# Optimization experiments

Measured on AMD Instinct MI355X. Metric: run time of the kernel, lower is better.

Reference implementation:

```python
import jax, jax.numpy as jnp
import numpy as np

B, N, DIM = 1, 2048, 2048
H, KVH = 32, 4                 # query heads, kv heads
D = DIM // H                   # head_dim = 64
REP = H // KVH                 # queries per kv = 8
KV_DIM = D * KVH               # 256


def _rope_tables(n, d, base=10000.0):
    inv = 1.0 / (base ** (np.arange(0, d, 2, dtype=np.float32) / d))
    t = np.arange(n, dtype=np.float32)
    freqs = np.outer(t, inv)                      # [n, d/2]
    emb = np.concatenate([freqs, freqs], axis=-1)  # [n, d]
    return jnp.asarray(np.cos(emb)), jnp.asarray(np.sin(emb))


def setup_inputs() -> dict:
    key = jax.random.key(0)
    ks = jax.random.split(key, 5)
    s = 0.02
    cos, sin = _rope_tables(N, D)
    return {
        "x": jax.random.normal(ks[0], (B, N, DIM), jnp.float32),
        "Wq": jax.random.normal(ks[1], (DIM, DIM), jnp.float32) * s,
        "Wk": jax.random.normal(ks[2], (KV_DIM, DIM), jnp.float32) * s,
        "Wv": jax.random.normal(ks[3], (KV_DIM, DIM), jnp.float32) * s,
        "Wo": jax.random.normal(ks[4], (DIM, DIM), jnp.float32) * s,
        "cos": cos,
        "sin": sin,
    }


def _rotate_half(t):
    d2 = t.shape[-1] // 2
    return jnp.concatenate([-t[..., d2:], t[..., :d2]], axis=-1)


def reference(x, Wq, Wk, Wv, Wo, cos, sin):
    b, n, _ = x.shape
    # projections (nn.Linear: x @ W.T)
    q = (x @ Wq.T).reshape(b, n, H, D).transpose(0, 2, 1, 3)     # b h n d
    k = (x @ Wk.T).reshape(b, n, KVH, D).transpose(0, 2, 1, 3)   # b g n d
    v = (x @ Wv.T).reshape(b, n, KVH, D).transpose(0, 2, 1, 3)
    # RoPE
    c = cos[None, None, :, :]
    s = sin[None, None, :, :]
    q = q * c + _rotate_half(q) * s
    k = k * c + _rotate_half(k) * s
    # expand KV heads (repeat_interleave over head dim)
    k = jnp.repeat(k, REP, axis=1)   # b h n d
    v = jnp.repeat(v, REP, axis=1)
    # causal attention with materialized scores (faithful to source)
    scale = 1.0 / jnp.sqrt(jnp.asarray(D, x.dtype))
    scores = jnp.einsum('bhld,bhsd->bhls', q, k) * scale
    causal = jnp.tril(jnp.ones((n, n), bool))
    scores = jnp.where(causal[None, None], scores, jnp.asarray(-jnp.inf, x.dtype))
    attn = jax.nn.softmax(scores, axis=-1)
    y = jnp.einsum('bhls,bhsd->bhld', attn, v)       # b h n d
    y = y.transpose(0, 2, 1, 3).reshape(b, n, DIM)   # b n (h d)
    return y @ Wo.T
```

## Files before the change

kernel.cpp:

```cpp
#include <hip/hip_runtime.h>

typedef unsigned short u16;
typedef __attribute__((ext_vector_type(8))) short short8;
typedef __attribute__((ext_vector_type(4))) float floatx4;

#define N_TOK 2048
#define DIM   2048
#define NH    32
#define NKVH  4
#define HD    64
#define KVD   256

#define OFF_X   0
#define OFF_WQ  4194304
#define OFF_WK  8388608
#define OFF_WV  8912896
#define OFF_WO  9437184
#define OFF_QP  13631488
#define OFF_KP  17825792
#define OFF_VP  18350080
#define OFF_YB  18874368

__device__ __forceinline__ float bf2f(u16 u) {
  union { unsigned i; float f; } c; c.i = ((unsigned)u) << 16; return c.f;
}
__device__ __forceinline__ u16 f2bf(float f) {
  union { float f; unsigned i; } c; c.f = f;
  unsigned x = c.i;
  return (u16)((x + 0x7fffu + ((x >> 16) & 1u)) >> 16);
}

__device__ __forceinline__ void gload16(const u16* g, u16* l) {
#if defined(__has_builtin) && __has_builtin(__builtin_amdgcn_global_load_lds)
  __builtin_amdgcn_global_load_lds(
      (const __attribute__((address_space(1))) void*)g,
      (__attribute__((address_space(3))) void*)l, 16, 0, 0);
#else
  *(short8*)l = *(const short8*)g;
#endif
}


__global__ __launch_bounds__(256) void cvt_pack(const float* __restrict__ x,
                                                const float* __restrict__ wq,
                                                const float* __restrict__ wk,
                                                const float* __restrict__ wv,
                                                const float* __restrict__ wo,
                                                u16* __restrict__ ws) {
  __shared__ __align__(16) u16 Ls[2048];
  const int tid = threadIdx.x;
  const int rfg = blockIdx.x >> 4;
  const int kcg = blockIdx.x & 15;
  const float* src; u16* dst; int lrf;
  if      (rfg < 128) { src = x;  dst = ws + OFF_X;  lrf = rfg; }
  else if (rfg < 256) { src = wq; dst = ws + OFF_WQ; lrf = rfg - 128; }
  else if (rfg < 272) { src = wk; dst = ws + OFF_WK; lrf = rfg - 256; }
  else if (rfg < 288) { src = wv; dst = ws + OFF_WV; lrf = rfg - 272; }
  else                { src = wo; dst = ws + OFF_WO; lrf = rfg - 288; }

  const int rr = tid >> 4, cb = tid & 15;
  const float* s = src + (size_t)(lrf * 16 + rr) * DIM + kcg * 128 + cb * 8;
  float4 v0 = ((const float4*)s)[0];
  float4 v1 = ((const float4*)s)[1];
  ushort4 o0, o1;
  o0.x = f2bf(v0.x); o0.y = f2bf(v0.y); o0.z = f2bf(v0.z); o0.w = f2bf(v0.w);
  o1.x = f2bf(v1.x); o1.y = f2bf(v1.y); o1.z = f2bf(v1.z); o1.w = f2bf(v1.w);
  const int ch = cb >> 2, qq = cb & 3;
  u16* lp = &Ls[ch * 512 + (qq * 16 + rr) * 8];
  ((ushort4*)lp)[0] = o0;
  ((ushort4*)lp)[1] = o1;
  __syncthreads();
  const int och = tid >> 6, lane = tid & 63;
  *(short8*)(dst + ((size_t)(lrf * 64 + kcg * 4 + och)) * 512 + lane * 8) =
      *(const short8*)&Ls[och * 512 + lane * 8];
}


__global__ __launch_bounds__(256) void gemm_qkv(const u16* __restrict__ xp,
                                                const u16* __restrict__ Wqp,
                                                const u16* __restrict__ Wkp,
                                                const u16* __restrict__ Wvp,
                                                const float* __restrict__ cs,
                                                const float* __restrict__ sn,
                                                u16* __restrict__ Qp,
                                                u16* __restrict__ Kp,
                                                u16* __restrict__ Vp) {
  __shared__ __align__(16) u16 As[8 * 512];
  __shared__ __align__(16) u16 Bs[16 * 512];
  const int tid  = threadIdx.x;
  const int lane = tid & 63;
  const int w    = tid >> 6;
  const int r    = lane & 15, q = lane >> 4;
  const int tm = blockIdx.x & 31;
  const int tn = blockIdx.x >> 5;
  const int wm = w & 1, wn = w >> 1;

  const u16* Wp; int rfB0;
  if (tn < 16)      { Wp = Wqp; rfB0 = tn * 8; }
  else if (tn < 18) { Wp = Wkp; rfB0 = (tn - 16) * 8; }
  else              { Wp = Wvp; rfB0 = (tn - 18) * 8; }
  const int rfA0 = tm * 4;

  const int cA0 = w, cA1 = w + 4;
  const u16* aS0 = xp + ((size_t)(rfA0 + (cA0 >> 1)) * 64 + (cA0 & 1)) * 512 + lane * 8;
  const u16* aS1 = xp + ((size_t)(rfA0 + (cA1 >> 1)) * 64 + (cA1 & 1)) * 512 + lane * 8;
  const u16* bS[4];
#pragma unroll
  for (int j = 0; j < 4; ++j) {
    int ch = w + 4 * j;
    bS[j] = Wp + ((size_t)(rfB0 + (ch >> 1)) * 64 + (ch & 1)) * 512 + lane * 8;
  }

  floatx4 acc[2][4];
#pragma unroll
  for (int a = 0; a < 2; ++a)
#pragma unroll
    for (int b = 0; b < 4; ++b) acc[a][b] = (floatx4){0.f, 0.f, 0.f, 0.f};

  for (int kc0 = 0; kc0 < 64; kc0 += 2) {
    const size_t ko = (size_t)kc0 * 512;
    __syncthreads();
    gload16(aS0 + ko, &As[cA0 * 512 + lane * 8]);
    gload16(aS1 + ko, &As[cA1 * 512 + lane * 8]);
#pragma unroll
    for (int j = 0; j < 4; ++j)
      gload16(bS[j] + ko, &Bs[(w + 4 * j) * 512 + lane * 8]);
    __syncthreads();

    short8 af[2][2], bf[4][2];
#pragma unroll
    for (int mi = 0; mi < 2; ++mi)
#pragma unroll
      for (int c = 0; c < 2; ++c)
        af[mi][c] = *(const short8*)&As[((wm * 2 + mi) * 2 + c) * 512 + lane * 8];
#pragma unroll
    for (int nj = 0; nj < 4; ++nj)
#pragma unroll
      for (int c = 0; c < 2; ++c)
        bf[nj][c] = *(const short8*)&Bs[((wn * 4 + nj) * 2 + c) * 512 + lane * 8];
#pragma unroll
    for (int c = 0; c < 2; ++c)
#pragma unroll
      for (int mi = 0; mi < 2; ++mi)
#pragma unroll
        for (int nj = 0; nj < 4; ++nj)
          acc[mi][nj] = __builtin_amdgcn_mfma_f32_16x16x32_bf16(af[mi][c], bf[nj][c], acc[mi][nj], 0, 0, 0);
  }

  if (tn < 18) {
    const int head = (tn < 16) ? (tn * 2 + wn) : ((tn - 16) * 2 + wn);
#pragma unroll
    for (int mi = 0; mi < 2; ++mi)
#pragma unroll
      for (int g = 0; g < 4; ++g) {
        int row = tm * 64 + wm * 32 + mi * 16 + 4 * q + g;
        const float* crow  = cs + (size_t)row * 64;
        const float* srow2 = sn + (size_t)row * 64;
#pragma unroll
        for (int nj = 0; nj < 2; ++nj) {
          int d = nj * 16 + r;
          float x0 = acc[mi][nj][g];
          float x1 = acc[mi][nj + 2][g];
          float o0 = x0 * crow[d]      - x1 * srow2[d];
          float o1 = x1 * crow[d + 32] + x0 * srow2[d + 32];
          int qq = d >> 3, j = d & 7;
          int lslot = (qq * 16 + (row & 15)) * 8 + j;
          if (tn < 16) {
            int sq = row >> 5, ii = (row >> 4) & 1;
            size_t base = ((size_t)(head * 64 + sq) * 4 + ii * 2) * 512 + lslot;
            Qp[base]       = f2bf(o0);
            Qp[base + 512] = f2bf(o1);
          } else {
            int kt2 = row >> 6, t = (row >> 4) & 3;
            size_t base = ((size_t)(head * 32 + kt2) * 8 + t * 2) * 512 + lslot;
            Kp[base]       = f2bf(o0);
            Kp[base + 512] = f2bf(o1);
          }
        }
      }
  } else {
#pragma unroll
    for (int mi = 0; mi < 2; ++mi)
#pragma unroll
      for (int nj = 0; nj < 4; ++nj) {
        int col  = (tn - 18) * 128 + wn * 64 + nj * 16 + r;
        int kvh  = col >> 6;
        int t    = (col & 63) >> 4;
        int rr   = col & 15;
        int row0 = tm * 64 + wm * 32 + mi * 16 + 4 * q;
        int kt2  = row0 >> 6;
        int wk   = row0 & 63;
        int s    = wk >> 5;
        int qq   = (wk & 31) >> 3;
        int j0   = wk & 7;
        uint2 pk;
        pk.x = (unsigned)f2bf(acc[mi][nj][0]) | ((unsigned)f2bf(acc[mi][nj][1]) << 16);
        pk.y = (unsigned)f2bf(acc[mi][nj][2]) | ((unsigned)f2bf(acc[mi][nj][3]) << 16);
        size_t idx = ((size_t)(kvh * 32 + kt2) * 8 + s * 4 + t) * 512 + (qq * 16 + rr) * 8 + j0;
        *(uint2*)(Vp + idx) = pk;
      }
  }
}

__global__ __launch_bounds__(256) void gemm_out(const u16* __restrict__ Ap,
                                                const u16* __restrict__ Wp,
                                                float* __restrict__ C) {
  __shared__ __align__(16) u16 As[8 * 512];
  __shared__ __align__(16) u16 Bs[16 * 512];
  const int tid  = threadIdx.x;
  const int lane = tid & 63;
  const int w    = tid >> 6;
  const int r    = lane & 15, q = lane >> 4;
  const int tn = blockIdx.x & 15;
  const int tm = blockIdx.x >> 4;
  const int wm = w & 1, wn = w >> 1;

  const int rfA0 = tm * 4, rfB0 = tn * 8;
  const int cA0 = w, cA1 = w + 4;
  const u16* aS0 = Ap + ((size_t)(rfA0 + (cA0 >> 1)) * 64 + (cA0 & 1)) * 512 + lane * 8;
  const u16* aS1 = Ap + ((size_t)(rfA0 + (cA1 >> 1)) * 64 + (cA1 & 1)) * 512 + lane * 8;
  const u16* bS[4];
#pragma unroll
  for (int j = 0; j < 4; ++j) {
    int ch = w + 4 * j;
    bS[j] = Wp + ((size_t)(rfB0 + (ch >> 1)) * 64 + (ch & 1)) * 512 + lane * 8;
  }

  floatx4 acc[2][4];
#pragma unroll
  for (int a = 0; a < 2; ++a)
#pragma unroll
    for (int b = 0; b < 4; ++b) acc[a][b] = (floatx4){0.f, 0.f, 0.f, 0.f};

  for (int kc0 = 0; kc0 < 64; kc0 += 2) {
    const size_t ko = (size_t)kc0 * 512;
    __syncthreads();
    gload16(aS0 + ko, &As[cA0 * 512 + lane * 8]);
    gload16(aS1 + ko, &As[cA1 * 512 + lane * 8]);
#pragma unroll
    for (int j = 0; j < 4; ++j)
      gload16(bS[j] + ko, &Bs[(w + 4 * j) * 512 + lane * 8]);
    __syncthreads();

    short8 af[2][2], bf[4][2];
#pragma unroll
    for (int mi = 0; mi < 2; ++mi)
#pragma unroll
      for (int c = 0; c < 2; ++c)
        af[mi][c] = *(const short8*)&As[((wm * 2 + mi) * 2 + c) * 512 + lane * 8];
#pragma unroll
    for (int nj = 0; nj < 4; ++nj)
#pragma unroll
      for (int c = 0; c < 2; ++c)
        bf[nj][c] = *(const short8*)&Bs[((wn * 4 + nj) * 2 + c) * 512 + lane * 8];
#pragma unroll
    for (int c = 0; c < 2; ++c)
#pragma unroll
      for (int mi = 0; mi < 2; ++mi)
#pragma unroll
        for (int nj = 0; nj < 4; ++nj)
          acc[mi][nj] = __builtin_amdgcn_mfma_f32_16x16x32_bf16(af[mi][c], bf[nj][c], acc[mi][nj], 0, 0, 0);
  }

#pragma unroll
  for (int mi = 0; mi < 2; ++mi)
#pragma unroll
    for (int g = 0; g < 4; ++g) {
      int row = tm * 64 + wm * 32 + mi * 16 + 4 * q + g;
#pragma unroll
      for (int nj = 0; nj < 4; ++nj)
        C[(size_t)row * DIM + tn * 128 + wn * 64 + nj * 16 + r] = acc[mi][nj][g];
    }
}

__global__ __launch_bounds__(128, 2) void attn_mfma(const u16* __restrict__ Qp,
                                                    const u16* __restrict__ Kp,
                                                    const u16* __restrict__ Vp,
                                                    u16* __restrict__ Ybp) {
  __shared__ __align__(16) u16 Pl[2][32][72];
  __shared__ float OcA[32][66];
  __shared__ float OcB[32][66];
  __shared__ float LcA[2][64], LcB[2][64];
  const int tid  = threadIdx.x;
  const int lane = tid & 63;
  const int w    = tid >> 6;
  const int r    = lane & 15;
  const int q    = lane >> 4;
  const int p    = blockIdx.x;
  const int h    = blockIdx.y;
  const int kvh  = h >> 3;
  const int jA   = 63 - p;
  const int jB   = p;
  const int baseqA = jA * 32, baseqB = jB * 32;
  const int tA = (jA >> 1) + 1, tB = (jB >> 1) + 1;
  const int ktmaxA = tA - 1, ktmaxB = tB - 1;

  short8 qfA[2][2], qfB[2][2];
#pragma unroll
  for (int i = 0; i < 2; ++i)
#pragma unroll
    for (int c = 0; c < 2; ++c) {
      qfA[i][c] = *(const short8*)(Qp + ((size_t)(h * 64 + jA) * 4 + i * 2 + c) * 512 + lane * 8);
      qfB[i][c] = *(const short8*)(Qp + ((size_t)(h * 64 + jB) * 4 + i * 2 + c) * 512 + lane * 8);
    }

  floatx4 OA[2][4], OB[2][4];
  float lsumA[2], lsumB[2];
#pragma unroll
  for (int i = 0; i < 2; ++i) {
    lsumA[i] = 0.f; lsumB[i] = 0.f;
#pragma unroll
    for (int t = 0; t < 4; ++t) {
      OA[i][t] = (floatx4){0.f, 0.f, 0.f, 0.f};
      OB[i][t] = (floatx4){0.f, 0.f, 0.f, 0.f};
    }
  }

  const u16* Kbase = Kp + (size_t)(kvh * 32) * 8 * 512;
  const u16* Vbase = Vp + (size_t)(kvh * 32) * 8 * 512;

  auto loadK = [&](int kt, short8 (&kf)[4][2]) {
    const u16* kb = Kbase + (size_t)kt * 8 * 512 + lane * 8;
#pragma unroll
    for (int t = 0; t < 4; ++t) {
      kf[t][0] = *(const short8*)(kb + (t * 2 + 0) * 512);
      kf[t][1] = *(const short8*)(kb + (t * 2 + 1) * 512);
    }
  };

  auto body = [&](int kt, int ktmax, int baseq,
                  short8 (&qf)[2][2], floatx4 (&O)[2][4], float (&lsum)[2],
                  short8 (&kc)[4][2], short8 (&kn)[4][2]) {
    short8 vb[2][4];
    {
      const u16* vbp = Vbase + (size_t)kt * 8 * 512 + lane * 8;
#pragma unroll
      for (int s = 0; s < 2; ++s)
#pragma unroll
        for (int t = 0; t < 4; ++t)
          vb[s][t] = *(const short8*)(vbp + (s * 4 + t) * 512);
    }

    loadK(kt + 2 <= ktmax ? kt + 2 : ktmax, kn);

    floatx4 ST[2][4];
#pragma unroll
    for (int i = 0; i < 2; ++i)
#pragma unroll
      for (int t = 0; t < 4; ++t) ST[i][t] = (floatx4){0.f, 0.f, 0.f, 0.f};
#pragma unroll
    for (int t = 0; t < 4; ++t)
#pragma unroll
      for (int i = 0; i < 2; ++i) {
        ST[i][t] = __builtin_amdgcn_mfma_f32_16x16x32_bf16(kc[t][0], qf[i][0], ST[i][t], 0, 0, 0);
        ST[i][t] = __builtin_amdgcn_mfma_f32_16x16x32_bf16(kc[t][1], qf[i][1], ST[i][t], 0, 0, 0);
      }

    if (kt == ktmax) {
#pragma unroll
      for (int i = 0; i < 2; ++i) {
        int qrow = baseq + 16 * i + r;
#pragma unroll
        for (int t = 0; t < 4; ++t) {
          int key = kt * 64 + 16 * t + 4 * q;
#pragma unroll
          for (int g = 0; g < 4; ++g)
            if (key + g > qrow) ST[i][t][g] = -1e30f;
        }
      }
    }

#pragma unroll
    for (int i = 0; i < 2; ++i)
#pragma unroll
      for (int t = 0; t < 4; ++t) {
        float p0 = __expf(0.125f * ST[i][t][0]);
        float p1 = __expf(0.125f * ST[i][t][1]);
        float p2 = __expf(0.125f * ST[i][t][2]);
        float p3 = __expf(0.125f * ST[i][t][3]);
        lsum[i] += (p0 + p1) + (p2 + p3);
        uint2 pk;
        pk.x = (unsigned)f2bf(p0) | ((unsigned)f2bf(p1) << 16);
        pk.y = (unsigned)f2bf(p2) | ((unsigned)f2bf(p3) << 16);
        *(uint2*)&Pl[w][16 * i + r][16 * t + 4 * q] = pk;
      }

#pragma unroll
    for (int s = 0; s < 2; ++s)
#pragma unroll
      for (int i = 0; i < 2; ++i) {
        short8 pa = *(const short8*)&Pl[w][16 * i + r][32 * s + 8 * q];
#pragma unroll
        for (int t = 0; t < 4; ++t)
          O[i][t] = __builtin_amdgcn_mfma_f32_16x16x32_bf16(pa, vb[s][t], O[i][t], 0, 0, 0);
      }
  };

  auto runloop = [&](int start, int ktmax, int baseq,
                     short8 (&qf)[2][2], floatx4 (&O)[2][4], float (&lsum)[2]) {
    if (start > ktmax) return;
    short8 kA[4][2], kB[4][2];
    loadK(start, kA);
    for (int kt = start; kt <= ktmax; kt += 4) {
      body(kt, ktmax, baseq, qf, O, lsum, kA, kB);
      if (kt + 2 <= ktmax) body(kt + 2, ktmax, baseq, qf, O, lsum, kB, kA);
    }
  };

  runloop(w, ktmaxA, baseqA, qfA, OA, lsumA);
  const int sB = (w + tA) & 1;
  runloop(sB, ktmaxB, baseqB, qfB, OB, lsumB);

  if (w == 1) {
#pragma unroll
    for (int i = 0; i < 2; ++i) {
#pragma unroll
      for (int t = 0; t < 4; ++t)
#pragma unroll
        for (int g = 0; g < 4; ++g)
          OcA[(i * 4 + t) * 4 + g][lane] = OA[i][t][g];
      LcA[i][lane] = lsumA[i];
    }
  } else {
#pragma unroll
    for (int i = 0; i < 2; ++i) {
#pragma unroll
      for (int t = 0; t < 4; ++t)
#pragma unroll
        for (int g = 0; g < 4; ++g)
          OcB[(i * 4 + t) * 4 + g][lane] = OB[i][t][g];
      LcB[i][lane] = lsumB[i];
    }
  }
  __syncthreads();

  auto finalize = [&](int baseq, floatx4 (&O)[2][4], float (&lsum)[2]) {
#pragma unroll
    for (int i = 0; i < 2; ++i) {
      lsum[i] += __shfl_xor(lsum[i], 16);
      lsum[i] += __shfl_xor(lsum[i], 32);
    }
#pragma unroll
    for (int i = 0; i < 2; ++i) {
      float inv[4];
#pragma unroll
      for (int g = 0; g < 4; ++g)
        inv[g] = 1.f / __shfl(lsum[i], 4 * q + g);
#pragma unroll
      for (int g = 0; g < 4; ++g) {
        int rowi = baseq + 16 * i + 4 * q + g;
        size_t rbase = ((size_t)(rowi >> 4) * 64 + h * 2) * 512 +
                       (((r >> 3)) * 16 + (rowi & 15)) * 8 + (r & 7);
        Ybp[rbase]       = f2bf(O[i][0][g] * inv[g]);
        Ybp[rbase + 256] = f2bf(O[i][1][g] * inv[g]);
        Ybp[rbase + 512] = f2bf(O[i][2][g] * inv[g]);
        Ybp[rbase + 768] = f2bf(O[i][3][g] * inv[g]);
      }
    }
  };

  if (w == 0) {
#pragma unroll
    for (int i = 0; i < 2; ++i) {
#pragma unroll
      for (int t = 0; t < 4; ++t)
#pragma unroll
        for (int g = 0; g < 4; ++g)
          OA[i][t][g] += OcA[(i * 4 + t) * 4 + g][lane];
      lsumA[i] += LcA[i][lane];
    }
    finalize(baseqA, OA, lsumA);
  } else {
#pragma unroll
    for (int i = 0; i < 2; ++i) {
#pragma unroll
      for (int t = 0; t < 4; ++t)
#pragma unroll
        for (int g = 0; g < 4; ++g)
          OB[i][t][g] += OcB[(i * 4 + t) * 4 + g][lane];
      lsumB[i] += LcB[i][lane];
    }
    finalize(baseqB, OB, lsumB);
  }
}

extern "C" void kernel_launch(void* const* d_in, const int* in_sizes, int n_in,
                              void* d_out, int out_size, void* d_ws, size_t ws_size,
                              hipStream_t stream) {
  const float* x  = (const float*)d_in[0];
  const float* Wq = (const float*)d_in[1];
  const float* Wk = (const float*)d_in[2];
  const float* Wv = (const float*)d_in[3];
  const float* Wo = (const float*)d_in[4];
  const float* cs = (const float*)d_in[5];
  const float* sn = (const float*)d_in[6];

  u16* ws  = (u16*)d_ws;
  u16* xp  = ws + OFF_X;
  u16* Wqp = ws + OFF_WQ;
  u16* Wkp = ws + OFF_WK;
  u16* Wvp = ws + OFF_WV;
  u16* Wop = ws + OFF_WO;
  u16* Qp  = ws + OFF_QP;
  u16* Kp  = ws + OFF_KP;
  u16* Vp  = ws + OFF_VP;
  u16* Ybp = ws + OFF_YB;

  cvt_pack<<<dim3(6656), 256, 0, stream>>>(x, Wq, Wk, Wv, Wo, ws);

  gemm_qkv<<<dim3(640), 256, 0, stream>>>(xp, Wqp, Wkp, Wvp, cs, sn, Qp, Kp, Vp);

  attn_mfma<<<dim3(32, 32), 128, 0, stream>>>(Qp, Kp, Vp, Ybp);

  gemm_out<<<dim3(512), 256, 0, stream>>>(Ybp, Wop, (float*)d_out);
}
```

Measured before the change: 192.1 us.

## Double-buffer LDS tiles in QKV and output GEMMs with async prefetch

Both projection GEMMs now keep two LDS buffers and issue global-to-LDS loads two k-steps ahead. Explicit vmcnt waits and raw s_barriers replace the paired __syncthreads, so memory latency can overlap with MFMA work. This doubles LDS use per block, which may lower occupancy, and it depends on the hand-counted vmcnt(6) matching the six loads issued per stage.

```diff
diff --git a/kernel.cpp b/kernel.cpp
--- a/kernel.cpp
+++ b/kernel.cpp
@@ -85,8 +85,8 @@
                                                 u16* __restrict__ Qp,
                                                 u16* __restrict__ Kp,
                                                 u16* __restrict__ Vp) {
-  __shared__ __align__(16) u16 As[8 * 512];
-  __shared__ __align__(16) u16 Bs[16 * 512];
+  __shared__ __align__(16) u16 As[2][8 * 512];
+  __shared__ __align__(16) u16 Bs[2][16 * 512];
   const int tid  = threadIdx.x;
   const int lane = tid & 63;
   const int w    = tid >> 6;
@@ -117,27 +117,35 @@
 #pragma unroll
     for (int b = 0; b < 4; ++b) acc[a][b] = (floatx4){0.f, 0.f, 0.f, 0.f};
 
-  for (int kc0 = 0; kc0 < 64; kc0 += 2) {
-    const size_t ko = (size_t)kc0 * 512;
-    __syncthreads();
-    gload16(aS0 + ko, &As[cA0 * 512 + lane * 8]);
-    gload16(aS1 + ko, &As[cA1 * 512 + lane * 8]);
+  auto stage = [&](int b, int kt) {
+    const size_t ko = (size_t)(kt * 2) * 512;
+    gload16(aS0 + ko, &As[b][cA0 * 512 + lane * 8]);
+    gload16(aS1 + ko, &As[b][cA1 * 512 + lane * 8]);
 #pragma unroll
     for (int j = 0; j < 4; ++j)
-      gload16(bS[j] + ko, &Bs[(w + 4 * j) * 512 + lane * 8]);
-    __syncthreads();
+      gload16(bS[j] + ko, &Bs[b][(w + 4 * j) * 512 + lane * 8]);
+  };
+
+  stage(0, 0);
+  stage(1, 1);
+  int cb = 0;
+  for (int kt = 0; kt < 32; ++kt) {
+    if (kt < 31) asm volatile("s_waitcnt vmcnt(6)" ::: "memory");
+    else         asm volatile("s_waitcnt vmcnt(0)" ::: "memory");
+    __builtin_amdgcn_s_barrier();
+    __builtin_amdgcn_sched_barrier(0);
 
     short8 af[2][2], bf[4][2];
 #pragma unroll
     for (int mi = 0; mi < 2; ++mi)
 #pragma unroll
       for (int c = 0; c < 2; ++c)
-        af[mi][c] = *(const short8*)&As[((wm * 2 + mi) * 2 + c) * 512 + lane * 8];
+        af[mi][c] = *(const short8*)&As[cb][((wm * 2 + mi) * 2 + c) * 512 + lane * 8];
 #pragma unroll
     for (int nj = 0; nj < 4; ++nj)
 #pragma unroll
       for (int c = 0; c < 2; ++c)
-        bf[nj][c] = *(const short8*)&Bs[((wn * 4 + nj) * 2 + c) * 512 + lane * 8];
+        bf[nj][c] = *(const short8*)&Bs[cb][((wn * 4 + nj) * 2 + c) * 512 + lane * 8];
 #pragma unroll
     for (int c = 0; c < 2; ++c)
 #pragma unroll
@@ -145,6 +153,11 @@
 #pragma unroll
         for (int nj = 0; nj < 4; ++nj)
           acc[mi][nj] = __builtin_amdgcn_mfma_f32_16x16x32_bf16(af[mi][c], bf[nj][c], acc[mi][nj], 0, 0, 0);
+
+    __builtin_amdgcn_sched_barrier(0);
+    __builtin_amdgcn_s_barrier();
+    if (kt + 2 < 32) stage(cb, kt + 2);
+    cb ^= 1;
   }
 
   if (tn < 18) {
@@ -205,8 +218,8 @@
 __global__ __launch_bounds__(256) void gemm_out(const u16* __restrict__ Ap,
                                                 const u16* __restrict__ Wp,
                                                 float* __restrict__ C) {
-  __shared__ __align__(16) u16 As[8 * 512];
-  __shared__ __align__(16) u16 Bs[16 * 512];
+  __shared__ __align__(16) u16 As[2][8 * 512];
+  __shared__ __align__(16) u16 Bs[2][16 * 512];
   const int tid  = threadIdx.x;
   const int lane = tid & 63;
   const int w    = tid >> 6;
@@ -232,27 +245,35 @@
 #pragma unroll
     for (int b = 0; b < 4; ++b) acc[a][b] = (floatx4){0.f, 0.f, 0.f, 0.f};
 
-  for (int kc0 = 0; kc0 < 64; kc0 += 2) {
-    const size_t ko = (size_t)kc0 * 512;
-    __syncthreads();
-    gload16(aS0 + ko, &As[cA0 * 512 + lane * 8]);
-    gload16(aS1 + ko, &As[cA1 * 512 + lane * 8]);
+  auto stage = [&](int b, int kt) {
+    const size_t ko = (size_t)(kt * 2) * 512;
+    gload16(aS0 + ko, &As[b][cA0 * 512 + lane * 8]);
+    gload16(aS1 + ko, &As[b][cA1 * 512 + lane * 8]);
 #pragma unroll
     for (int j = 0; j < 4; ++j)
-      gload16(bS[j] + ko, &Bs[(w + 4 * j) * 512 + lane * 8]);
-    __syncthreads();
+      gload16(bS[j] + ko, &Bs[b][(w + 4 * j) * 512 + lane * 8]);
+  };
+
+  stage(0, 0);
+  stage(1, 1);
+  int cb = 0;
+  for (int kt = 0; kt < 32; ++kt) {
+    if (kt < 31) asm volatile("s_waitcnt vmcnt(6)" ::: "memory");
+    else         asm volatile("s_waitcnt vmcnt(0)" ::: "memory");
+    __builtin_amdgcn_s_barrier();
+    __builtin_amdgcn_sched_barrier(0);
 
     short8 af[2][2], bf[4][2];
 #pragma unroll
     for (int mi = 0; mi < 2; ++mi)
 #pragma unroll
       for (int c = 0; c < 2; ++c)
-        af[mi][c] = *(const short8*)&As[((wm * 2 + mi) * 2 + c) * 512 + lane * 8];
+        af[mi][c] = *(const short8*)&As[cb][((wm * 2 + mi) * 2 + c) * 512 + lane * 8];
 #pragma unroll
     for (int nj = 0; nj < 4; ++nj)
 #pragma unroll
       for (int c = 0; c < 2; ++c)
-        bf[nj][c] = *(const short8*)&Bs[((wn * 4 + nj) * 2 + c) * 512 + lane * 8];
+        bf[nj][c] = *(const short8*)&Bs[cb][((wn * 4 + nj) * 2 + c) * 512 + lane * 8];
 #pragma unroll
     for (int c = 0; c < 2; ++c)
 #pragma unroll
@@ -260,6 +281,11 @@
 #pragma unroll
         for (int nj = 0; nj < 4; ++nj)
           acc[mi][nj] = __builtin_amdgcn_mfma_f32_16x16x32_bf16(af[mi][c], bf[nj][c], acc[mi][nj], 0, 0, 0);
+
+    __builtin_amdgcn_sched_barrier(0);
+    __builtin_amdgcn_s_barrier();
+    if (kt + 2 < 32) stage(cb, kt + 2);
+    cb ^= 1;
   }
 
 #pragma unroll
```

After: 191.3 us (median of 2 runs). Within noise of the previous version (-0.4%).
